# Performance work log

Measured on AMD Instinct MI355X. Metric: run time of the kernel, lower is better.

## Reference

```python
import jax, jax.numpy as jnp
import numpy as np

O_NODES = 50000
N_EDGES = 200000
D = 256          # per-object feature dim (input_dim[0] == output_dim[0])
HIDDEN = 512
CONST = 10.0     # self-confidence constant from the module


def setup_inputs() -> dict:
    key = jax.random.key(0)
    k1, k2, k3, k4, k5 = jax.random.split(key, 5)
    object_feats = jax.random.normal(k1, (O_NODES, D), dtype=jnp.float32)
    pairs = jax.random.randint(k2, (N_EDGES, 2), 0, O_NODES, dtype=jnp.int64)
    confidence = jax.random.normal(k3, (N_EDGES,), dtype=jnp.float32)
    # MLP: Linear(2D -> HIDDEN), ReLU, Linear(HIDDEN -> 2D), kaiming-style scale
    W1 = jax.random.normal(k4, (2 * D, HIDDEN), dtype=jnp.float32) * jnp.sqrt(2.0 / (2 * D))
    b1 = jnp.zeros((HIDDEN,), dtype=jnp.float32)
    W2 = jax.random.normal(k5, (HIDDEN, 2 * D), dtype=jnp.float32) * jnp.sqrt(2.0 / HIDDEN)
    b2 = jnp.zeros((2 * D,), dtype=jnp.float32)
    return {"object_feats": object_feats, "pairs": pairs, "confidence": confidence,
            "W1": W1, "b1": b1, "W2": W2, "b2": b2}


def reference(object_feats, pairs, confidence, W1, b1, W2, b2):
    n_nodes, d = object_feats.shape
    sub = pairs[:, 0]
    obj = pairs[:, 1]
    # gather pair features and run the edge MLP
    feats = jnp.concatenate([object_feats[sub], object_feats[obj]], axis=1)  # (R, 2D)
    h = jax.nn.relu(feats @ W1 + b1)
    out = h @ W2 + b2                                                        # (R, 2D)
    sub_feat = out[:, :d]
    obj_feat = out[:, d:]
    # scatter: each edge contributes sub_feat to node sub, obj_feat to node obj,
    # each with logit = confidence; every node also has its own feat with logit CONST.
    seg = jnp.concatenate([sub, obj])                 # (2R,)
    vals = jnp.concatenate([sub_feat, obj_feat], 0)   # (2R, D)
    confs = jnp.concatenate([confidence, confidence])  # (2R,)
    # numerically stable segment softmax (self entry included in the max)
    m_edges = jax.ops.segment_max(confs, seg, num_segments=n_nodes)
    m = jnp.maximum(m_edges, CONST)
    w = jnp.exp(confs - m[seg])
    self_w = jnp.exp(CONST - m)                        # (N,)
    denom = jax.ops.segment_sum(w, seg, num_segments=n_nodes) + self_w
    numer = jax.ops.segment_sum(w[:, None] * vals, seg, num_segments=n_nodes) \
            + self_w[:, None] * object_feats
    new_feats = numer / denom[:, None]
    # nodes with no incident edges reduce to softmax([CONST]) -> identity, matching
    # the original (which leaves nodes > pairs.max() untouched).
    return new_feats
```

## Files before the change

### kernel.cpp

```cpp
#include <hip/hip_runtime.h>
#include <hip/hip_bf16.h>
#include <hip/hip_fp8.h>

#define O_NODES 50000
#define N_EDGES 200000
#define DD 256
#define S_SLOTS 32
#define OVF_CAP 4096

typedef float f32x4 __attribute__((ext_vector_type(4)));

__device__ __forceinline__ unsigned pack4_fp8(float a, float b, float c, float d) {
#if __has_builtin(__builtin_amdgcn_cvt_pk_fp8_f32)
    int v = __builtin_amdgcn_cvt_pk_fp8_f32(a, b, 0, false);
    v = __builtin_amdgcn_cvt_pk_fp8_f32(c, d, v, true);
    return (unsigned)v;
#else
    __hip_fp8_e4m3 x(a), y(b), z(c), w(d);
    return (unsigned)x.__x | ((unsigned)y.__x << 8) | ((unsigned)z.__x << 16) | ((unsigned)w.__x << 24);
#endif
}

__device__ __forceinline__ unsigned char f2fp8(float x) {
#if __has_builtin(__builtin_amdgcn_cvt_pk_fp8_f32)
    return (unsigned char)(__builtin_amdgcn_cvt_pk_fp8_f32(x, x, 0, false) & 0xff);
#else
    __hip_fp8_e4m3 t(x); return t.__x;
#endif
}

__device__ __forceinline__ f32x4 unpack4_fp8(unsigned v) {
#if __has_builtin(__builtin_amdgcn_cvt_pk_f32_fp8)
    auto lo = __builtin_amdgcn_cvt_pk_f32_fp8((int)v, false);
    auto hi = __builtin_amdgcn_cvt_pk_f32_fp8((int)v, true);
    return (f32x4){lo[0], lo[1], hi[0], hi[1]};
#else
    __hip_fp8_e4m3 t0, t1, t2, t3;
    t0.__x = v & 0xff; t1.__x = (v >> 8) & 0xff; t2.__x = (v >> 16) & 0xff; t3.__x = (v >> 24) & 0xff;
    return (f32x4){(float)t0, (float)t1, (float)t2, (float)t3};
#endif
}

__device__ __forceinline__ f32x4 mfma_fp8(long a, long b, f32x4 c) {
    return __builtin_amdgcn_mfma_f32_16x16x32_fp8_fp8(a, b, c, 0, 0, 0);
}

__device__ __forceinline__ int get_pair(const int* __restrict__ p, long e, int which, int is32) {
    return is32 ? p[2 * e + which] : p[4 * e + 2 * which];
}

__device__ __forceinline__ float load_f(const void* p, long i, int is_f32) {
    if (is_f32) return ((const float*)p)[i];
    unsigned short u = ((const unsigned short*)p)[i];
    return __uint_as_float((unsigned)u << 16);
}

__device__ __forceinline__ float bf2f(unsigned short u) {
    return __uint_as_float((unsigned)u << 16);
}

__device__ __forceinline__ unsigned short f2bf(float x) {
    __hip_bfloat16 h = __float2bfloat16(x);
    return *(unsigned short*)&h;
}

__device__ __forceinline__ int detect_is32_w(const int* __restrict__ pairs) {
    int lane = threadIdx.x & 63;
    unsigned long long m = __ballot(pairs[2 * lane + 1] != 0);
    return m != 0ull;
}
__device__ __forceinline__ int detect_isf_w(const unsigned short* __restrict__ w) {
    int lane = threadIdx.x & 63;
    unsigned short u = w[2 * lane];
    float v = fabsf(__uint_as_float((unsigned)u << 16));
    unsigned long long m = __ballot(v > 0.004f && v < 16.0f);
    return (__popcll(m) < 32) ? 1 : 0;
}

#define MEGA_A 12500
#define MEGA_B 2048
#define MEGA_C 782
__global__ __launch_bounds__(256) void mega_setup(
    const void* __restrict__ objf, const int* __restrict__ pairs, const void* __restrict__ conf,
    const void* __restrict__ W1, const void* __restrict__ W2,
    const void* __restrict__ b1, const void* __restrict__ b2,
    unsigned* __restrict__ objf8, unsigned char* __restrict__ w1p, unsigned char* __restrict__ w2p,
    float* __restrict__ b1f, float* __restrict__ b2f,
    float* __restrict__ mbuf, int* __restrict__ count, int* __restrict__ flag,
    int2* __restrict__ inc2, int4* __restrict__ ovf)
{
    int b = blockIdx.x, t = threadIdx.x;
    if (b < MEGA_A) {
        int isf = detect_isf_w((const unsigned short*)objf);
        int i4 = b * 256 + t;
        float x0, x1, x2, x3;
        if (isf) {
            float4 v = ((const float4*)objf)[i4];
            x0 = v.x; x1 = v.y; x2 = v.z; x3 = v.w;
        } else {
            ushort4 u = ((const ushort4*)objf)[i4];
            x0 = bf2f(u.x); x1 = bf2f(u.y); x2 = bf2f(u.z); x3 = bf2f(u.w);
        }
        objf8[i4] = pack4_fp8(x0, x1, x2, x3);
    } else if (b < MEGA_A + MEGA_B) {
        int isf = detect_isf_w((const unsigned short*)objf);
        int bb = b - MEGA_A;
        int idx = ((bb & 1023) << 8) + t;
        if (bb < 1024) {
            int j = idx & 7, half = (idx >> 3) & 1, lane = (idx >> 4) & 63;
            int p = (idx >> 10) & 31, tk = idx >> 15;
            int k = tk * 32 + (lane >> 4) * 8 + j;
            int n = (2 * p + half) * 16 + (lane & 15);
            long src = (n < 512) ? ((long)k * 512 + n) : ((long)(256 + k) * 512 + (n - 512));
            w1p[idx] = f2fp8(load_f(W1, src, isf));
        } else {
            int j = idx & 7, half = (idx >> 3) & 1, lane = (idx >> 4) & 63;
            int p = (idx >> 10) & 7, tk = idx >> 13;
            int k = tk * 32 + (lane >> 4) * 8 + j;
            int n = (2 * p + half) * 16 + (lane & 15);
            long src = (k < 512) ? ((long)k * 512 + n) : ((long)(k - 512) * 512 + 256 + n);
            w2p[idx] = f2fp8(load_f(W2, src, isf));
        }
    } else if (b < MEGA_A + MEGA_B + MEGA_C) {
        int is32 = detect_is32_w(pairs);
        int isf  = detect_isf_w((const unsigned short*)objf);
        int i = (b - MEGA_A - MEGA_B) * 256 + t;
        if (i >= N_EDGES) return;
        int s = get_pair(pairs, i, 0, is32);
        int o = get_pair(pairs, i, 1, is32);
        float c = load_f(conf, i, isf);
        int cb = __float_as_int(c);
        atomicMax((int*)&mbuf[s], cb);
        atomicMax((int*)&mbuf[o], cb);
        int idx_s = atomicAdd(&count[s], 1);
        int rec_s = (o << 1) | 0;
        if (idx_s < S_SLOTS) inc2[(long)s * S_SLOTS + idx_s] = make_int2(rec_s, cb);
        else { int oi = atomicAdd(&flag[2], 1); if (oi < OVF_CAP) ovf[oi] = make_int4(s, rec_s, cb, 0); }
        int idx_o = atomicAdd(&count[o], 1);
        int rec_o = (s << 1) | 1;
        if (idx_o < S_SLOTS) inc2[(long)o * S_SLOTS + idx_o] = make_int2(rec_o, cb);
        else { int oi = atomicAdd(&flag[2], 1); if (oi < OVF_CAP) ovf[oi] = make_int4(o, rec_o, cb, 0); }
    } else if (b == MEGA_A + MEGA_B + MEGA_C) {
        int isf = detect_isf_w((const unsigned short*)objf);
        b1f[t]       = load_f(b1, t, isf);
        b1f[256 + t] = load_f(b1, 256 + t, isf);
        b2f[t]       = load_f(b2, t, isf);
        b2f[256 + t] = load_f(b2, 256 + t, isf);
    } else {
        int is32 = detect_is32_w(pairs);
        int isf  = detect_isf_w((const unsigned short*)objf);
        if (t == 0) { flag[0] = is32; flag[1] = isf; }
    }
}

__global__ __launch_bounds__(512, 4) void gemm1_node(
    const unsigned* __restrict__ objf8,
    const unsigned char* __restrict__ w1p,
    unsigned char* __restrict__ P)
{
    extern __shared__ char smem[];
    unsigned char* sA = (unsigned char*)smem;

    const int tid  = threadIdx.x;
    const int wave = tid >> 6;
    const int lane = tid & 63;
    const int l15  = lane & 15;
    const int lq   = lane >> 4;
    const int mb   = blockIdx.x >> 1;
    const int nh   = blockIdx.x & 1;
    const long bs  = (long)mb * 64;

    #pragma unroll
    for (int it = 0; it < 4; ++it) {
        int q   = it * 512 + tid;
        int m15 = q & 15;
        int mtp = (q >> 4) & 1;
        int h   = (q >> 5) & 1;
        int lqk = (q >> 6) & 3;
        int tk  = (q >> 8) & 7;
        int m   = (h * 2 + mtp) * 16 + m15;
        long node = bs + m; if (node >= O_NODES) node = O_NODES - 1;
        uint2 v = *(const uint2*)(objf8 + node * 64 + tk * 8 + lqk * 2);
        *(uint2*)(sA + h * 8192 + (tk * 64 + lqk * 16 + m15) * 16 + mtp * 8) = v;
    }
    __syncthreads();

    f32x4 acc[4][4];
    #pragma unroll
    for (int mt = 0; mt < 4; ++mt)
        #pragma unroll
        for (int nt = 0; nt < 4; ++nt)
            acc[mt][nt] = (f32x4){0.f, 0.f, 0.f, 0.f};

    {
        const ulonglong2* bq = (const ulonglong2*)w1p;
        const int pbase = nh * 16 + wave * 2;
        #pragma unroll 2
        for (int tk = 0; tk < 8; ++tk) {
            ulonglong2 av01 = *(const ulonglong2*)(sA + tk * 1024 + lane * 16);
            ulonglong2 av23 = *(const ulonglong2*)(sA + 8192 + tk * 1024 + lane * 16);
            ulonglong2 b01  = bq[(tk * 32 + pbase) * 64 + lane];
            ulonglong2 b23  = bq[(tk * 32 + pbase + 1) * 64 + lane];
            long a0 = (long)av01.x, a1 = (long)av01.y;
            long a2 = (long)av23.x, a3 = (long)av23.y;
            acc[0][0] = mfma_fp8(a0, (long)b01.x, acc[0][0]);
            acc[1][0] = mfma_fp8(a1, (long)b01.x, acc[1][0]);
            acc[2][0] = mfma_fp8(a2, (long)b01.x, acc[2][0]);
            acc[3][0] = mfma_fp8(a3, (long)b01.x, acc[3][0]);
            acc[0][1] = mfma_fp8(a0, (long)b01.y, acc[0][1]);
            acc[1][1] = mfma_fp8(a1, (long)b01.y, acc[1][1]);
            acc[2][1] = mfma_fp8(a2, (long)b01.y, acc[2][1]);
            acc[3][1] = mfma_fp8(a3, (long)b01.y, acc[3][1]);
            acc[0][2] = mfma_fp8(a0, (long)b23.x, acc[0][2]);
            acc[1][2] = mfma_fp8(a1, (long)b23.x, acc[1][2]);
            acc[2][2] = mfma_fp8(a2, (long)b23.x, acc[2][2]);
            acc[3][2] = mfma_fp8(a3, (long)b23.x, acc[3][2]);
            acc[0][3] = mfma_fp8(a0, (long)b23.y, acc[0][3]);
            acc[1][3] = mfma_fp8(a1, (long)b23.y, acc[1][3]);
            acc[2][3] = mfma_fp8(a2, (long)b23.y, acc[2][3]);
            acc[3][3] = mfma_fp8(a3, (long)b23.y, acc[3][3]);
        }
    }
    __syncthreads();

    #pragma unroll
    for (int nt = 0; nt < 4; ++nt) {
        int c = wave * 64 + nt * 16 + l15;
        #pragma unroll
        for (int mt = 0; mt < 4; ++mt) {
            #pragma unroll
            for (int r = 0; r < 4; ++r) {
                sA[(mt * 16 + lq * 4 + r) * 528 + c] = f2fp8(acc[mt][nt][r]);
            }
        }
    }
    __syncthreads();
    #pragma unroll
    for (int it = 0; it < 4; ++it) {
        int idx = it * 512 + tid;
        int row = idx >> 5;
        int ch  = idx & 31;
        if (bs + row < O_NODES) {
            uint4 v = *(const uint4*)(sA + row * 528 + ch * 16);
            ((uint4*)P)[(bs + row) * 64 + nh * 32 + ch] = v;
        }
    }
}

__global__ __launch_bounds__(256) void node_accum(
    const unsigned* __restrict__ Pu,
    const int2* __restrict__ inc2,
    const int* __restrict__ count,
    const float* __restrict__ mbuf,
    const int* __restrict__ flag,
    const int4* __restrict__ ovf,
    const float4* __restrict__ b1f4,
    unsigned* __restrict__ Hcat_u,
    float* __restrict__ ws_s, float* __restrict__ ws_o)
{
    const int wv    = threadIdx.x >> 6;
    const int hw    = wv & 1;
    const int lane  = threadIdx.x & 63;
    const int slice = blockIdx.x * 2 + (wv >> 1);
    const int nbase = slice * 8;

    int cq = 0; float mq = 0.f;
    if (lane < 8) { cq = count[nbase + lane]; mq = mbuf[nbase + lane]; }

    float4 bq = b1f4[hw * 64 + lane];
    f32x4 b1v = {bq.x, bq.y, bq.z, bq.w};

    const long slotbase = (long)nbase * S_SLOTS;
    const long prow0    = (long)nbase * 256;

    int2 rec = inc2[slotbase + lane];
    unsigned st0 = Pu[prow0 +       hw * 64 + lane];
    unsigned sb0 = Pu[prow0 + 128 + hw * 64 + lane];
    unsigned st1 = Pu[prow0 + 256 + hw * 64 + lane];
    unsigned sb1 = Pu[prow0 + 384 + hw * 64 + lane];

    #pragma unroll 1
    for (int p = 0; p < 4; ++p) {
        const int n0 = nbase + 2 * p;
        int2 rec_n = make_int2(0, 0);
        unsigned stA = 0, sbA = 0, stB = 0, sbB = 0;
        if (p < 3) {
            rec_n = inc2[slotbase + (p + 1) * 64 + lane];
            long prw = (long)(n0 + 2) * 256;
            stA = Pu[prw +       hw * 64 + lane];
            sbA = Pu[prw + 128 + hw * 64 + lane];
            stB = Pu[prw + 256 + hw * 64 + lane];
            sbB = Pu[prw + 384 + hw * 64 + lane];
        }
        float mml = __shfl(mq, 2 * p + (lane >> 5), 64);
        float wl  = __expf(__int_as_float(rec.y) - mml);
        int   prl = rec.x;

        #pragma unroll
        for (int half = 0; half < 2; ++half) {
            const int n = n0 + half;
            const int deg = __shfl(cq, 2 * p + half, 64);
            const float mm = __shfl(mq, 2 * p + half, 64);
            const unsigned stc = half ? st1 : st0;
            const unsigned sbc = half ? sb1 : sb0;
            f32x4 ot = unpack4_fp8(stc), ob = unpack4_fp8(sbc);
            f32x4 accS = {0.f, 0.f, 0.f, 0.f}, accO = {0.f, 0.f, 0.f, 0.f};
            float wS = 0.f, wO = 0.f;
            const int lb = half * 32;
            const int nb = deg < S_SLOTS ? deg : S_SLOTS;
            int i = 0;
            while (i < nb) {
                int kb = nb - i; if (kb > 8) kb = 8;
                unsigned pv[8]; float wk[8]; int rl[8];
                #pragma unroll
                for (int k = 0; k < 8; ++k) if (k < kb) {
                    int prk = __shfl(prl, lb + i + k, 64);
                    wk[k] = __shfl(wl, lb + i + k, 64);
                    rl[k] = prk & 1;
                    pv[k] = Pu[(long)(prk >> 1) * 256 + (rl[k] ? 0 : 128) + hw * 64 + lane];
                }
                #pragma unroll
                for (int k = 0; k < 8; ++k) if (k < kb) {
                    f32x4 pp = unpack4_fp8(pv[k]);
                    float wkk = wk[k];
                    if (rl[k]) {
                        wO += wkk;
                        #pragma unroll
                        for (int j = 0; j < 4; ++j) accO[j] += wkk * fmaxf(ob[j] + pp[j] + b1v[j], 0.f);
                    } else {
                        wS += wkk;
                        #pragma unroll
                        for (int j = 0; j < 4; ++j) accS[j] += wkk * fmaxf(ot[j] + pp[j] + b1v[j], 0.f);
                    }
                }
                i += kb;
            }
            if (deg > S_SLOTS) {
                int no = flag[2]; if (no > OVF_CAP) no = OVF_CAP;
                for (int tt = 0; tt < no; ++tt) {
                    int4 o = ovf[tt];
                    if (o.x == n) {
                        int role = o.y & 1, partner = o.y >> 1;
                        float wv = __expf(__int_as_float(o.z) - mm);
                        unsigned pvv = Pu[(long)partner * 256 + (role ? 0 : 128) + hw * 64 + lane];
                        f32x4 pp = unpack4_fp8(pvv);
                        if (role) {
                            wO += wv;
                            #pragma unroll
                            for (int j = 0; j < 4; ++j) accO[j] += wv * fmaxf(ob[j] + pp[j] + b1v[j], 0.f);
                        } else {
                            wS += wv;
                            #pragma unroll
                            for (int j = 0; j < 4; ++j) accS[j] += wv * fmaxf(ot[j] + pp[j] + b1v[j], 0.f);
                        }
                    }
                }
            }
            long prow = (long)n * 256;
            Hcat_u[prow +       hw * 64 + lane] = pack4_fp8(accS[0], accS[1], accS[2], accS[3]);
            Hcat_u[prow + 128 + hw * 64 + lane] = pack4_fp8(accO[0], accO[1], accO[2], accO[3]);
            if (hw == 0 && lane == 0) { ws_s[n] = wS; ws_o[n] = wO; }
        }
        if (p < 3) { rec = rec_n; st0 = stA; sb0 = sbA; st1 = stB; sb1 = sbB; }
    }
}

__global__ __launch_bounds__(512, 4) void gemm2_node(
    const unsigned* __restrict__ Hcat,
    const unsigned char* __restrict__ w2p,
    const float* __restrict__ mbuf,
    const float* __restrict__ ws_s, const float* __restrict__ ws_o,
    const void* __restrict__ objf, const float* __restrict__ b2f,
    void* __restrict__ out, const int* __restrict__ flag)
{
    extern __shared__ char smem[];
    unsigned char* sA = (unsigned char*)smem;
    float* sS    = (float*)(smem + 32768);
    float* sSelf = sS + 64;
    float* sInv  = sS + 128;
    float* sWs   = sS + 192;
    float* sWo   = sS + 256;

    const int tid  = threadIdx.x;
    const int wave = tid >> 6;
    const int lane = tid & 63;
    const int l15  = lane & 15;
    const int lq   = lane >> 4;
    const long bs  = (long)blockIdx.x * 64;
    const int isf  = flag[1];

    if (tid < 64) {
        long node = bs + tid; if (node >= O_NODES) node = O_NODES - 1;
        float mm = mbuf[node];
        float mn = fmaxf(mm, 10.0f);
        float S     = __expf(mm - mn);
        float selfw = __expf(10.0f - mn);
        float wss = ws_s[node], wso = ws_o[node];
        sS[tid] = S; sSelf[tid] = selfw; sWs[tid] = wss; sWo[tid] = wso;
        sInv[tid] = 1.0f / (S * (wss + wso) + selfw);
    }

    f32x4 acc[4][2];
    #pragma unroll
    for (int mt = 0; mt < 4; ++mt)
        #pragma unroll
        for (int nt = 0; nt < 2; ++nt)
            acc[mt][nt] = (f32x4){0.f, 0.f, 0.f, 0.f};

    const ulonglong2* bq = (const ulonglong2*)w2p;
    #pragma unroll
    for (int kh = 0; kh < 2; ++kh) {
        #pragma unroll
        for (int it = 0; it < 8; ++it) {
            int q   = it * 512 + tid;
            int m15 = q & 15;
            int mtp = (q >> 4) & 1;
            int h   = (q >> 5) & 1;
            int lqk = (q >> 6) & 3;
            int tk  = (q >> 8) & 15;
            int m   = (h * 2 + mtp) * 16 + m15;
            long node = bs + m; if (node >= O_NODES) node = O_NODES - 1;
            uint2 v = *(const uint2*)(Hcat + node * 256 + kh * 128 + tk * 8 + lqk * 2);
            *(uint2*)(sA + h * 16384 + (tk * 64 + lqk * 16 + m15) * 16 + mtp * 8) = v;
        }
        __syncthreads();
        #pragma unroll 2
        for (int tk = 0; tk < 16; ++tk) {
            int kt = kh * 16 + tk;
            ulonglong2 av01 = *(const ulonglong2*)(sA + tk * 1024 + lane * 16);
            ulonglong2 av23 = *(const ulonglong2*)(sA + 16384 + tk * 1024 + lane * 16);
            ulonglong2 b    = bq[(kt * 8 + wave) * 64 + lane];
            long a0 = (long)av01.x, a1 = (long)av01.y;
            long a2 = (long)av23.x, a3 = (long)av23.y;
            acc[0][0] = mfma_fp8(a0, (long)b.x, acc[0][0]);
            acc[1][0] = mfma_fp8(a1, (long)b.x, acc[1][0]);
            acc[2][0] = mfma_fp8(a2, (long)b.x, acc[2][0]);
            acc[3][0] = mfma_fp8(a3, (long)b.x, acc[3][0]);
            acc[0][1] = mfma_fp8(a0, (long)b.y, acc[0][1]);
            acc[1][1] = mfma_fp8(a1, (long)b.y, acc[1][1]);
            acc[2][1] = mfma_fp8(a2, (long)b.y, acc[2][1]);
            acc[3][1] = mfma_fp8(a3, (long)b.y, acc[3][1]);
        }
        __syncthreads();
    }

    #pragma unroll
    for (int nt = 0; nt < 2; ++nt) {
        int c = wave * 32 + nt * 16 + l15;
        float b2c = b2f[c];
        float b2d = b2f[256 + c];
        #pragma unroll
        for (int mt = 0; mt < 4; ++mt) {
            #pragma unroll
            for (int r = 0; r < 4; ++r) {
                int row = mt * 16 + lq * 4 + r;
                long node = bs + row;
                if (node < O_NODES) {
                    float o = load_f(objf, node * 256 + c, isf);
                    float val = (sS[row] * (acc[mt][nt][r] + sWs[row] * b2c + sWo[row] * b2d)
                                 + sSelf[row] * o) * sInv[row];
                    if (isf) ((float*)out)[node * 256 + c] = val;
                    else     ((unsigned short*)out)[node * 256 + c] = f2bf(val);
                }
            }
        }
    }
}

extern "C" void kernel_launch(void* const* d_in, const int* in_sizes, int n_in,
                              void* d_out, int out_size, void* d_ws, size_t ws_size,
                              hipStream_t stream) {
    const void* objf  = d_in[0];
    const int*  pairs = (const int*)d_in[1];
    const void* conf  = d_in[2];
    const void* W1    = d_in[3];
    const void* b1    = d_in[4];
    const void* W2    = d_in[5];
    const void* b2    = d_in[6];

    char* ws = (char*)d_ws;
    int*   count   = (int*)  ws;
    float* mbuf    = (float*)(ws + 200000);
    int*   flag    = (int*)  (ws + 400000);
    int4*  ovf     = (int4*) (ws + 400064);
    unsigned char* w1p = (unsigned char*)(ws + 465600);
    unsigned char* w2p = (unsigned char*)(ws + 727744);
    float* wss     = (float*)(ws + 989888);
    float* wso     = (float*)(ws + 1189888);
    float* b1f     = (float*)(ws + 1389888);
    float* b2f     = (float*)(ws + 1391936);
    int2*  inc2    = (int2*) (ws + 1393984);
    unsigned char* P     = (unsigned char*)(ws + 14193984);
    unsigned*      objf8 = (unsigned*)(ws + 65393984);
    unsigned char* Hcat  = (unsigned char*)(ws + 65393984);

    hipMemsetAsync(count, 0, 400064, stream);

    mega_setup<<<MEGA_A + MEGA_B + MEGA_C + 2, 256, 0, stream>>>(
        objf, pairs, conf, W1, W2, b1, b2, objf8, w1p, w2p, b1f, b2f,
        mbuf, count, flag, inc2, ovf);

    gemm1_node<<<2 * ((O_NODES + 63) / 64), 512, 33792, stream>>>(objf8, w1p, P);

    node_accum<<<O_NODES / 16, 256, 0, stream>>>(
        (const unsigned*)P, inc2, count, mbuf, flag, ovf, (const float4*)b1f,
        (unsigned*)Hcat, wss, wso);

    gemm2_node<<<(O_NODES + 63) / 64, 512, 34048, stream>>>(
        (const unsigned*)Hcat, w2p, mbuf, wss, wso, objf, b2f, d_out, flag);
}
```

Before: 312.7 us.

## Fuse fp8 conversion into gemm1 and precompute exp weights in edge setup

Drops the separate pass that converted the node features to fp8 in the setup kernel. gemm1 now reads fp32/bf16 features directly and packs them to fp8 while staging into LDS, so the extra fp8 feature buffer is never written or read back. The edge setup now clamps confidence and stores exp(c) per record, and node_accum multiplies by exp(-max) instead of computing an exp per edge. node_accum is also restructured to process one node per iteration, loading records as vectors straight from memory instead of through cross-lane shuffles. The risks are that gemm1 reads the wider source data twice (once per N-half block), and that the split exponent can lose precision or overflow for large logits.

After: 308.7 us. Within noise of the previous version (-1.3%).

```diff
diff --git a/kernel.cpp b/kernel.cpp
--- a/kernel.cpp
+++ b/kernel.cpp
@@ -77,36 +77,22 @@
     return (__popcll(m) < 32) ? 1 : 0;
 }
 
-#define MEGA_A 12500
 #define MEGA_B 2048
 #define MEGA_C 782
 __global__ __launch_bounds__(256) void mega_setup(
     const void* __restrict__ objf, const int* __restrict__ pairs, const void* __restrict__ conf,
     const void* __restrict__ W1, const void* __restrict__ W2,
     const void* __restrict__ b1, const void* __restrict__ b2,
-    unsigned* __restrict__ objf8, unsigned char* __restrict__ w1p, unsigned char* __restrict__ w2p,
+    unsigned char* __restrict__ w1p, unsigned char* __restrict__ w2p,
     float* __restrict__ b1f, float* __restrict__ b2f,
     float* __restrict__ mbuf, int* __restrict__ count, int* __restrict__ flag,
     int2* __restrict__ inc2, int4* __restrict__ ovf)
 {
     int b = blockIdx.x, t = threadIdx.x;
-    if (b < MEGA_A) {
+    if (b < MEGA_B) {
         int isf = detect_isf_w((const unsigned short*)objf);
-        int i4 = b * 256 + t;
-        float x0, x1, x2, x3;
-        if (isf) {
-            float4 v = ((const float4*)objf)[i4];
-            x0 = v.x; x1 = v.y; x2 = v.z; x3 = v.w;
-        } else {
-            ushort4 u = ((const ushort4*)objf)[i4];
-            x0 = bf2f(u.x); x1 = bf2f(u.y); x2 = bf2f(u.z); x3 = bf2f(u.w);
-        }
-        objf8[i4] = pack4_fp8(x0, x1, x2, x3);
-    } else if (b < MEGA_A + MEGA_B) {
-        int isf = detect_isf_w((const unsigned short*)objf);
-        int bb = b - MEGA_A;
-        int idx = ((bb & 1023) << 8) + t;
-        if (bb < 1024) {
+        int idx = ((b & 1023) << 8) + t;
+        if (b < 1024) {
             int j = idx & 7, half = (idx >> 3) & 1, lane = (idx >> 4) & 63;
             int p = (idx >> 10) & 31, tk = idx >> 15;
             int k = tk * 32 + (lane >> 4) * 8 + j;
@@ -121,26 +107,28 @@
             long src = (k < 512) ? ((long)k * 512 + n) : ((long)(k - 512) * 512 + 256 + n);
             w2p[idx] = f2fp8(load_f(W2, src, isf));
         }
-    } else if (b < MEGA_A + MEGA_B + MEGA_C) {
+    } else if (b < MEGA_B + MEGA_C) {
         int is32 = detect_is32_w(pairs);
         int isf  = detect_isf_w((const unsigned short*)objf);
-        int i = (b - MEGA_A - MEGA_B) * 256 + t;
+        int i = (b - MEGA_B) * 256 + t;
         if (i >= N_EDGES) return;
         int s = get_pair(pairs, i, 0, is32);
         int o = get_pair(pairs, i, 1, is32);
         float c = load_f(conf, i, isf);
+        c = fminf(fmaxf(c, -80.f), 80.f);
         int cb = __float_as_int(c);
+        int eb = __float_as_int(__expf(c));
         atomicMax((int*)&mbuf[s], cb);
         atomicMax((int*)&mbuf[o], cb);
         int idx_s = atomicAdd(&count[s], 1);
         int rec_s = (o << 1) | 0;
-        if (idx_s < S_SLOTS) inc2[(long)s * S_SLOTS + idx_s] = make_int2(rec_s, cb);
-        else { int oi = atomicAdd(&flag[2], 1); if (oi < OVF_CAP) ovf[oi] = make_int4(s, rec_s, cb, 0); }
+        if (idx_s < S_SLOTS) inc2[(long)s * S_SLOTS + idx_s] = make_int2(rec_s, eb);
+        else { int oi = atomicAdd(&flag[2], 1); if (oi < OVF_CAP) ovf[oi] = make_int4(s, rec_s, eb, 0); }
         int idx_o = atomicAdd(&count[o], 1);
         int rec_o = (s << 1) | 1;
-        if (idx_o < S_SLOTS) inc2[(long)o * S_SLOTS + idx_o] = make_int2(rec_o, cb);
-        else { int oi = atomicAdd(&flag[2], 1); if (oi < OVF_CAP) ovf[oi] = make_int4(o, rec_o, cb, 0); }
-    } else if (b == MEGA_A + MEGA_B + MEGA_C) {
+        if (idx_o < S_SLOTS) inc2[(long)o * S_SLOTS + idx_o] = make_int2(rec_o, eb);
+        else { int oi = atomicAdd(&flag[2], 1); if (oi < OVF_CAP) ovf[oi] = make_int4(o, rec_o, eb, 0); }
+    } else if (b == MEGA_B + MEGA_C) {
         int isf = detect_isf_w((const unsigned short*)objf);
         b1f[t]       = load_f(b1, t, isf);
         b1f[256 + t] = load_f(b1, 256 + t, isf);
@@ -154,12 +142,14 @@
 }
 
 __global__ __launch_bounds__(512, 4) void gemm1_node(
-    const unsigned* __restrict__ objf8,
+    const void* __restrict__ objf,
     const unsigned char* __restrict__ w1p,
     unsigned char* __restrict__ P)
 {
     extern __shared__ char smem[];
     unsigned char* sA = (unsigned char*)smem;
+
+    const int isf = detect_isf_w((const unsigned short*)objf);
 
     const int tid  = threadIdx.x;
     const int wave = tid >> 6;
@@ -180,7 +170,19 @@
         int tk  = (q >> 8) & 7;
         int m   = (h * 2 + mtp) * 16 + m15;
         long node = bs + m; if (node >= O_NODES) node = O_NODES - 1;
-        uint2 v = *(const uint2*)(objf8 + node * 64 + tk * 8 + lqk * 2);
+        long f4 = node * 64 + tk * 8 + lqk * 2;
+        uint2 v;
+        if (isf) {
+            float4 a = ((const float4*)objf)[f4];
+            float4 c = ((const float4*)objf)[f4 + 1];
+            v.x = pack4_fp8(a.x, a.y, a.z, a.w);
+            v.y = pack4_fp8(c.x, c.y, c.z, c.w);
+        } else {
+            ushort4 a = ((const ushort4*)objf)[f4];
+            ushort4 c = ((const ushort4*)objf)[f4 + 1];
+            v.x = pack4_fp8(bf2f(a.x), bf2f(a.y), bf2f(a.z), bf2f(a.w));
+            v.y = pack4_fp8(bf2f(c.x), bf2f(c.y), bf2f(c.z), bf2f(c.w));
+        }
         *(uint2*)(sA + h * 8192 + (tk * 64 + lqk * 16 + m15) * 16 + mtp * 8) = v;
     }
     __syncthreads();
@@ -258,110 +260,101 @@
     unsigned* __restrict__ Hcat_u,
     float* __restrict__ ws_s, float* __restrict__ ws_o)
 {
-    const int wv    = threadIdx.x >> 6;
-    const int hw    = wv & 1;
-    const int lane  = threadIdx.x & 63;
-    const int slice = blockIdx.x * 2 + (wv >> 1);
-    const int nbase = slice * 8;
-
-    int cq = 0; float mq = 0.f;
-    if (lane < 8) { cq = count[nbase + lane]; mq = mbuf[nbase + lane]; }
-
-    float4 bq = b1f4[hw * 64 + lane];
-    f32x4 b1v = {bq.x, bq.y, bq.z, bq.w};
-
-    const long slotbase = (long)nbase * S_SLOTS;
-    const long prow0    = (long)nbase * 256;
-
-    int2 rec = inc2[slotbase + lane];
-    unsigned st0 = Pu[prow0 +       hw * 64 + lane];
-    unsigned sb0 = Pu[prow0 + 128 + hw * 64 + lane];
-    unsigned st1 = Pu[prow0 + 256 + hw * 64 + lane];
-    unsigned sb1 = Pu[prow0 + 384 + hw * 64 + lane];
+    const int lane = threadIdx.x & 63;
+    const int hw   = (threadIdx.x >> 6) & 1;
+    const int nbase = __builtin_amdgcn_readfirstlane(
+        (blockIdx.x * 2 + (threadIdx.x >> 7)) * 8);
+
+    float4 bqv = b1f4[hw * 64 + lane];
+    f32x4 b1v = {bqv.x, bqv.y, bqv.z, bqv.w};
+    const int col = hw * 64 + lane;
+
+    unsigned st = Pu[(long)nbase * 256 + col];
+    unsigned sb = Pu[(long)nbase * 256 + 128 + col];
 
     #pragma unroll 1
-    for (int p = 0; p < 4; ++p) {
-        const int n0 = nbase + 2 * p;
-        int2 rec_n = make_int2(0, 0);
-        unsigned stA = 0, sbA = 0, stB = 0, sbB = 0;
-        if (p < 3) {
-            rec_n = inc2[slotbase + (p + 1) * 64 + lane];
-            long prw = (long)(n0 + 2) * 256;
-            stA = Pu[prw +       hw * 64 + lane];
-            sbA = Pu[prw + 128 + hw * 64 + lane];
-            stB = Pu[prw + 256 + hw * 64 + lane];
-            sbB = Pu[prw + 384 + hw * 64 + lane];
-        }
-        float mml = __shfl(mq, 2 * p + (lane >> 5), 64);
-        float wl  = __expf(__int_as_float(rec.y) - mml);
-        int   prl = rec.x;
-
+    for (int t = 0; t < 8; ++t) {
+        const int n = nbase + t;
+        const int deg = count[n];
+        const float mm = mbuf[n];
+        const float emm = __expf(-mm);
+        const int2* srec = inc2 + (long)n * S_SLOTS;
+        int4 r0 = *(const int4*)(srec);
+        int4 r1 = *(const int4*)(srec + 2);
+        int4 r2 = *(const int4*)(srec + 4);
+        int4 r3 = *(const int4*)(srec + 6);
+        unsigned stn = 0, sbn = 0;
+        if (t < 7) {
+            stn = Pu[(long)(n + 1) * 256 + col];
+            sbn = Pu[(long)(n + 1) * 256 + 128 + col];
+        }
+        f32x4 ots = unpack4_fp8(st), obs = unpack4_fp8(sb);
+        f32x4 otb, obb;
         #pragma unroll
-        for (int half = 0; half < 2; ++half) {
-            const int n = n0 + half;
-            const int deg = __shfl(cq, 2 * p + half, 64);
-            const float mm = __shfl(mq, 2 * p + half, 64);
-            const unsigned stc = half ? st1 : st0;
-            const unsigned sbc = half ? sb1 : sb0;
-            f32x4 ot = unpack4_fp8(stc), ob = unpack4_fp8(sbc);
-            f32x4 accS = {0.f, 0.f, 0.f, 0.f}, accO = {0.f, 0.f, 0.f, 0.f};
-            float wS = 0.f, wO = 0.f;
-            const int lb = half * 32;
-            const int nb = deg < S_SLOTS ? deg : S_SLOTS;
-            int i = 0;
-            while (i < nb) {
-                int kb = nb - i; if (kb > 8) kb = 8;
-                unsigned pv[8]; float wk[8]; int rl[8];
+        for (int j = 0; j < 4; ++j) { otb[j] = ots[j] + b1v[j]; obb[j] = obs[j] + b1v[j]; }
+
+        f32x4 accS = {0.f, 0.f, 0.f, 0.f}, accO = {0.f, 0.f, 0.f, 0.f};
+        float wS = 0.f, wO = 0.f;
+
+        auto ACC = [&](int rx, int ry, unsigned pv) {
+            float wk = __int_as_float(ry) * emm;
+            f32x4 pp = unpack4_fp8(pv);
+            if (rx & 1) {
+                wO += wk;
                 #pragma unroll
-                for (int k = 0; k < 8; ++k) if (k < kb) {
-                    int prk = __shfl(prl, lb + i + k, 64);
-                    wk[k] = __shfl(wl, lb + i + k, 64);
-                    rl[k] = prk & 1;
-                    pv[k] = Pu[(long)(prk >> 1) * 256 + (rl[k] ? 0 : 128) + hw * 64 + lane];
-                }
+                for (int j = 0; j < 4; ++j) accO[j] += wk * fmaxf(obb[j] + pp[j], 0.f);
+            } else {
+                wS += wk;
                 #pragma unroll
-                for (int k = 0; k < 8; ++k) if (k < kb) {
-                    f32x4 pp = unpack4_fp8(pv[k]);
-                    float wkk = wk[k];
-                    if (rl[k]) {
-                        wO += wkk;
-                        #pragma unroll
-                        for (int j = 0; j < 4; ++j) accO[j] += wkk * fmaxf(ob[j] + pp[j] + b1v[j], 0.f);
-                    } else {
-                        wS += wkk;
-                        #pragma unroll
-                        for (int j = 0; j < 4; ++j) accS[j] += wkk * fmaxf(ot[j] + pp[j] + b1v[j], 0.f);
-                    }
-                }
-                i += kb;
+                for (int j = 0; j < 4; ++j) accS[j] += wk * fmaxf(otb[j] + pp[j], 0.f);
             }
-            if (deg > S_SLOTS) {
-                int no = flag[2]; if (no > OVF_CAP) no = OVF_CAP;
-                for (int tt = 0; tt < no; ++tt) {
-                    int4 o = ovf[tt];
-                    if (o.x == n) {
-                        int role = o.y & 1, partner = o.y >> 1;
-                        float wv = __expf(__int_as_float(o.z) - mm);
-                        unsigned pvv = Pu[(long)partner * 256 + (role ? 0 : 128) + hw * 64 + lane];
-                        f32x4 pp = unpack4_fp8(pvv);
-                        if (role) {
-                            wO += wv;
-                            #pragma unroll
-                            for (int j = 0; j < 4; ++j) accO[j] += wv * fmaxf(ob[j] + pp[j] + b1v[j], 0.f);
-                        } else {
-                            wS += wv;
-                            #pragma unroll
-                            for (int j = 0; j < 4; ++j) accS[j] += wv * fmaxf(ot[j] + pp[j] + b1v[j], 0.f);
-                        }
-                    }
+        };
+
+        const int nb = deg < S_SLOTS ? deg : S_SLOTS;
+        for (int i = 0; i < nb; i += 8) {
+            int kb = nb - i; if (kb > 8) kb = 8;
+            if (i) {
+                r0 = *(const int4*)(srec + i);
+                r1 = *(const int4*)(srec + i + 2);
+                r2 = *(const int4*)(srec + i + 4);
+                r3 = *(const int4*)(srec + i + 6);
+            }
+            if (kb == 8) {
+                unsigned p0 = Pu[(long)(r0.x >> 1) * 256 + ((r0.x & 1) ? 0 : 128) + col];
+                unsigned p1 = Pu[(long)(r0.z >> 1) * 256 + ((r0.z & 1) ? 0 : 128) + col];
+                unsigned p2 = Pu[(long)(r1.x >> 1) * 256 + ((r1.x & 1) ? 0 : 128) + col];
+                unsigned p3 = Pu[(long)(r1.z >> 1) * 256 + ((r1.z & 1) ? 0 : 128) + col];
+                unsigned p4 = Pu[(long)(r2.x >> 1) * 256 + ((r2.x & 1) ? 0 : 128) + col];
+                unsigned p5 = Pu[(long)(r2.z >> 1) * 256 + ((r2.z & 1) ? 0 : 128) + col];
+                unsigned p6 = Pu[(long)(r3.x >> 1) * 256 + ((r3.x & 1) ? 0 : 128) + col];
+                unsigned p7 = Pu[(long)(r3.z >> 1) * 256 + ((r3.z & 1) ? 0 : 128) + col];
+                ACC(r0.x, r0.y, p0); ACC(r0.z, r0.w, p1);
+                ACC(r1.x, r1.y, p2); ACC(r1.z, r1.w, p3);
+                ACC(r2.x, r2.y, p4); ACC(r2.z, r2.w, p5);
+                ACC(r3.x, r3.y, p6); ACC(r3.z, r3.w, p7);
+            } else {
+                for (int k = 0; k < kb; ++k) {
+                    int2 rr = srec[i + k];
+                    unsigned pv = Pu[(long)(rr.x >> 1) * 256 + ((rr.x & 1) ? 0 : 128) + col];
+                    ACC(rr.x, rr.y, pv);
                 }
             }
-            long prow = (long)n * 256;
-            Hcat_u[prow +       hw * 64 + lane] = pack4_fp8(accS[0], accS[1], accS[2], accS[3]);
-            Hcat_u[prow + 128 + hw * 64 + lane] = pack4_fp8(accO[0], accO[1], accO[2], accO[3]);
-            if (hw == 0 && lane == 0) { ws_s[n] = wS; ws_o[n] = wO; }
-        }
-        if (p < 3) { rec = rec_n; st0 = stA; sb0 = sbA; st1 = stB; sb1 = sbB; }
+        }
+        if (deg > S_SLOTS) {
+            int no = flag[2]; if (no > OVF_CAP) no = OVF_CAP;
+            for (int tt = 0; tt < no; ++tt) {
+                int4 o = ovf[tt];
+                if (o.x == n) {
+                    unsigned pv = Pu[(long)(o.y >> 1) * 256 + ((o.y & 1) ? 0 : 128) + col];
+                    ACC(o.y, o.z, pv);
+                }
+            }
+        }
+        long hrow = (long)n * 256;
+        Hcat_u[hrow + col]       = pack4_fp8(accS[0], accS[1], accS[2], accS[3]);
+        Hcat_u[hrow + 128 + col] = pack4_fp8(accO[0], accO[1], accO[2], accO[3]);
+        if (hw == 0 && lane == 0) { ws_s[n] = wS; ws_o[n] = wO; }
+        st = stn; sb = sbn;
     }
 }
 
@@ -491,16 +484,15 @@
     float* b2f     = (float*)(ws + 1391936);
     int2*  inc2    = (int2*) (ws + 1393984);
     unsigned char* P     = (unsigned char*)(ws + 14193984);
-    unsigned*      objf8 = (unsigned*)(ws + 65393984);
     unsigned char* Hcat  = (unsigned char*)(ws + 65393984);
 
     hipMemsetAsync(count, 0, 400064, stream);
 
-    mega_setup<<<MEGA_A + MEGA_B + MEGA_C + 2, 256, 0, stream>>>(
-        objf, pairs, conf, W1, W2, b1, b2, objf8, w1p, w2p, b1f, b2f,
+    mega_setup<<<MEGA_B + MEGA_C + 2, 256, 0, stream>>>(
+        objf, pairs, conf, W1, W2, b1, b2, w1p, w2p, b1f, b2f,
         mbuf, count, flag, inc2, ovf);
 
-    gemm1_node<<<2 * ((O_NODES + 63) / 64), 512, 33792, stream>>>(objf8, w1p, P);
+    gemm1_node<<<2 * ((O_NODES + 63) / 64), 512, 33792, stream>>>(objf, w1p, P);
 
     node_accum<<<O_NODES / 16, 256, 0, stream>>>(
         (const unsigned*)P, inc2, count, mbuf, flag, ovf, (const float4*)b1f,
```
